# Kernel tuning notes

Hardware: AMD Instinct MI355X
Metric: run time of the kernel (lower is better)

## Reference

```python
import jax, jax.numpy as jnp
import numpy as np

B, T, C, H = 4, 2048, 1024, 16
HD = C // H  # head dim = 64


def setup_inputs() -> dict:
    key = jax.random.key(0)
    ks = jax.random.split(key, 8)
    s = 1.0 / np.sqrt(C)
    return {
        "x": jax.random.normal(ks[0], (B, T, C), dtype=jnp.float32),
        "Wq": jax.random.normal(ks[1], (C, C), dtype=jnp.float32) * s,
        "bq": jax.random.normal(ks[2], (C,), dtype=jnp.float32) * 0.02,
        "Wk": jax.random.normal(ks[3], (C, C), dtype=jnp.float32) * s,
        "bk": jax.random.normal(ks[4], (C,), dtype=jnp.float32) * 0.02,
        "Wv": jax.random.normal(ks[5], (C, C), dtype=jnp.float32) * s,
        "bv": jax.random.normal(ks[6], (C,), dtype=jnp.float32) * 0.02,
        "Wp": jax.random.normal(ks[7], (C, C), dtype=jnp.float32) * s,
    }


def reference(x, Wq, bq, Wk, bk, Wv, bv, Wp):
    # Separate Q/K/V projections (torch Linear: y = x @ W.T + b)
    q = jnp.einsum("btc,dc->btd", x, Wq) + bq
    k = jnp.einsum("btc,dc->btd", x, Wk) + bk
    v = jnp.einsum("btc,dc->btd", x, Wv) + bv
    # split heads -> [B, H, T, HD]
    q = q.reshape(B, T, H, HD).transpose(0, 2, 1, 3)
    k = k.reshape(B, T, H, HD).transpose(0, 2, 1, 3)
    v = v.reshape(B, T, H, HD).transpose(0, 2, 1, 3)
    # causal scaled dot-product attention
    scale = 1.0 / np.sqrt(HD)
    scores = jnp.einsum("bhqd,bhkd->bhqk", q, k) * scale
    causal_mask = jnp.tril(jnp.ones((T, T), dtype=bool))  # [T, T]
    scores = jnp.where(causal_mask, scores, jnp.finfo(scores.dtype).min)
    att = jax.nn.softmax(scores, axis=-1)
    y = jnp.einsum("bhqk,bhkd->bhqd", att, v)
    # merge heads and output projection (no bias)
    y = y.transpose(0, 2, 1, 3).reshape(B, T, C)
    return jnp.einsum("btc,dc->btd", y, Wp)
```

## Files before the change

kernel.cpp:

```cpp
#include <hip/hip_runtime.h>
#include <stdint.h>


typedef unsigned short u16;
typedef short bf16x8 __attribute__((ext_vector_type(8)));
typedef float f32x4  __attribute__((ext_vector_type(4)));

#define LOG2E 1.4426950408889634f
#define CSHIFT 8.0f

__device__ __forceinline__ void gload_lds16(const void* g, void* l) {
  __builtin_amdgcn_global_load_lds(
      (const __attribute__((address_space(1))) void*)g,
      (__attribute__((address_space(3))) void*)l,
      16, 0, 0);
}

__device__ __forceinline__ u16 f2bf(float f) {
  union { float f; uint32_t u; } v; v.f = f;
  uint32_t u = v.u;
  u += 0x7fffu + ((u >> 16) & 1u);
  return (u16)(u >> 16);
}

__device__ __forceinline__ uint32_t pack_bf16(float a, float b) {
#if __has_builtin(__builtin_amdgcn_cvt_pk_bf16_f32)
  typedef short v2s __attribute__((ext_vector_type(2)));
  v2s r = __builtin_amdgcn_cvt_pk_bf16_f32(a, b);
  union { v2s s; uint32_t u; } c; c.s = r;
  return c.u;
#else
  return (uint32_t)f2bf(a) | ((uint32_t)f2bf(b) << 16);
#endif
}

__device__ __forceinline__ float fexp2(float x) {
#if __has_builtin(__builtin_amdgcn_exp2f)
  return __builtin_amdgcn_exp2f(x);
#else
  return exp2f(x);
#endif
}

__device__ __forceinline__ float frcp(float x) {
#if __has_builtin(__builtin_amdgcn_rcpf)
  return __builtin_amdgcn_rcpf(x);
#else
  return 1.0f / x;
#endif
}

__global__ void cvt_all_kernel(const float* __restrict__ x,
                               const float* __restrict__ w0,
                               const float* __restrict__ w1,
                               const float* __restrict__ w2,
                               const float* __restrict__ w3,
                               uint4* __restrict__ out) {
  int i = blockIdx.x * blockDim.x + threadIdx.x;
  if (i >= 1572864) return;
  const float* src;
  int local;
  if (i < 1048576) { src = x; local = i; }
  else {
    int j = i - 1048576;
    int seg = j >> 17;
    local = j & 131071;
    src = (seg == 0) ? w0 : (seg == 1) ? w1 : (seg == 2) ? w2 : w3;
  }
  const int blk = local >> 9, s = local & 511;
  const int tile = blk >> 5, ks = blk & 31;
  const int r = s >> 6, ln = s & 63;
  const int row = tile * 128 + r * 16 + (ln & 15);
  const int col = ks * 32 + (ln >> 4) * 8;
  const float4* p = (const float4*)(src + (size_t)row * 1024 + col);
  const float4 v0 = p[0], v1 = p[1];
  uint4 pk;
  pk.x = pack_bf16(v0.x, v0.y); pk.y = pack_bf16(v0.z, v0.w);
  pk.z = pack_bf16(v1.x, v1.y); pk.w = pack_bf16(v1.z, v1.w);
  out[i] = pk;
}

__global__ __launch_bounds__(256, 3) void gemm_qkv(
    const u16* __restrict__ A,
    const u16* __restrict__ Wq, const u16* __restrict__ Wk, const u16* __restrict__ Wv,
    const float* __restrict__ bq, const float* __restrict__ bk, const float* __restrict__ bv,
    u16* __restrict__ Qo, u16* __restrict__ Ko, u16* __restrict__ Vo) {
  __shared__ __attribute__((aligned(16))) u16 shm[24576];
  const int tid = threadIdx.x;
  const int wv = tid >> 6, lane = tid & 63;
  const int cl = lane & 15, quad = lane >> 4;
  const int m0 = blockIdx.x * 128;
  const int mat = blockIdx.y >> 3;
  const int nt0 = blockIdx.y & 7;
  const int n0 = nt0 * 128;
  const int wm = (wv >> 1) * 64, wn = (wv & 1) * 64;
  const u16* W = (mat == 0) ? Wq : (mat == 1) ? Wk : Wv;
  const float* bias = (mat == 0) ? bq : (mat == 1) ? bk : bv;

  const u16* Abase = A + ((size_t)blockIdx.x << 17);
  const u16* Wbase = W + ((size_t)nt0 << 17);

  auto stage = [&](int buf, int ks) {
    const u16* a = Abase + ((size_t)ks << 12);
    const u16* w = Wbase + ((size_t)ks << 12);
    u16* la = &shm[buf * 4096];
    u16* lb = &shm[12288 + buf * 4096];
    gload_lds16(a + tid * 8,        la + tid * 8);
    gload_lds16(a + 2048 + tid * 8, la + 2048 + tid * 8);
    gload_lds16(w + tid * 8,        lb + tid * 8);
    gload_lds16(w + 2048 + tid * 8, lb + 2048 + tid * 8);
  };

  f32x4 acc[4][4] = {};

  stage(0, 0);
  stage(1, 1);

  for (int kt = 0; kt < 32; ++kt) {
    if (kt < 31) {
      asm volatile("s_waitcnt vmcnt(4)" ::: "memory");
    } else {
      asm volatile("s_waitcnt vmcnt(0)" ::: "memory");
    }
    __builtin_amdgcn_s_barrier();
    if (kt < 30) stage((kt + 2) % 3, kt + 2);
    const int buf = kt % 3;
    const u16* la = &shm[buf * 4096];
    const u16* lb = &shm[12288 + buf * 4096];
    bf16x8 af[4], bfr[4];
#pragma unroll
    for (int i = 0; i < 4; i++)
      af[i] = *(const bf16x8*)&la[(((wm >> 4) + i) * 64 + lane) * 8];
#pragma unroll
    for (int j = 0; j < 4; j++)
      bfr[j] = *(const bf16x8*)&lb[(((wn >> 4) + j) * 64 + lane) * 8];
#pragma unroll
    for (int i = 0; i < 4; i++)
#pragma unroll
      for (int j = 0; j < 4; j++)
        acc[i][j] = __builtin_amdgcn_mfma_f32_16x16x32_bf16(af[i], bfr[j], acc[i][j], 0, 0, 0);
  }

  __syncthreads();
  u16* etile = shm;

  if (mat == 2) {
#pragma unroll
    for (int j = 0; j < 4; j++) {
      const int n_loc = wn + j * 16 + cl;
      const float bj = bias[n0 + n_loc];
      const int hh = n_loc >> 6, hd = n_loc & 63;
#pragma unroll
      for (int i = 0; i < 4; i++) {
        const int tb = wm + i * 16 + quad * 4;
        uint2 pk;
        pk.x = pack_bf16(acc[i][j][0] + bj, acc[i][j][1] + bj);
        pk.y = pack_bf16(acc[i][j][2] + bj, acc[i][j][3] + bj);
        const int off = ((hd >> 4) * 4 + ((tb >> 5) & 3)) * 512
                      + (((tb >> 3) & 3) * 16 + (hd & 15)) * 8 + (tb & 7);
        *(uint2*)&etile[hh * 8192 + off] = pk;
      }
    }
  } else if (mat == 1) {
#pragma unroll
    for (int j = 0; j < 4; j++) {
      const int n_loc = wn + j * 16 + cl;
      const float bj = bias[n0 + n_loc];
      const int hh = n_loc >> 6, hd = n_loc & 63;
      const int rlo = hd >> 5, lhi = ((hd >> 3) & 3) * 16, e = hd & 7;
#pragma unroll
      for (int i = 0; i < 4; i++) {
#pragma unroll
        for (int r = 0; r < 4; r++) {
          const int tl = wm + i * 16 + quad * 4 + r;
          const int off = (((tl >> 4) & 7) * 2 + rlo) * 512 + (lhi + (tl & 15)) * 8 + e;
          etile[hh * 8192 + off] = f2bf(acc[i][j][r] + bj);
        }
      }
    }
  } else {
    const float sc = 0.125f * LOG2E;
#pragma unroll
    for (int j = 0; j < 4; j++) {
      const int n_loc = wn + j * 16 + cl;
      const float bj = bias[n0 + n_loc];
      const int hh = n_loc >> 6, hd = n_loc & 63;
#pragma unroll
      for (int i = 0; i < 4; i++) {
#pragma unroll
        for (int r = 0; r < 4; r++) {
          const int tl = wm + i * 16 + quad * 4 + r;
          etile[hh * 8192 + tl * 64 + hd] = f2bf((acc[i][j][r] + bj) * sc);
        }
      }
    }
  }
  __syncthreads();

  const int b = m0 >> 11, t0 = m0 & 2047;
  const int h0 = n0 >> 6;
  if (mat == 0) {
#pragma unroll
    for (int p = 0; p < 8; ++p) {
      const int idx = p * 2048 + tid * 8;
      const int hh = idx >> 13, off = idx & 8191;
      u16* dst = Qo + ((size_t)(b * 16 + h0 + hh) * 2048 + t0) * 64 + off;
      *(uint4*)dst = *(const uint4*)&etile[idx];
    }
  } else {
    u16* base = (mat == 1) ? Ko : Vo;
    const int kt = t0 >> 7;
#pragma unroll
    for (int p = 0; p < 8; ++p) {
      const int idx = p * 2048 + tid * 8;
      const int hh = idx >> 13, off = idx & 8191;
      u16* dst = base + ((size_t)(b * 16 + h0 + hh) << 17) + ((size_t)kt << 13) + off;
      *(uint4*)dst = *(const uint4*)&etile[idx];
    }
  }
}

__global__ __launch_bounds__(256, 3) void gemm_out(
    const u16* __restrict__ A, const u16* __restrict__ W,
    float* __restrict__ out) {
  __shared__ __attribute__((aligned(16))) u16 shm[24576];
  const int tid = threadIdx.x;
  const int wv = tid >> 6, lane = tid & 63;
  const int cl = lane & 15, quad = lane >> 4;
  const int m0 = blockIdx.x * 128;
  const int n0 = blockIdx.y * 128;
  const int wm = (wv >> 1) * 64, wn = (wv & 1) * 64;

  const u16* Abase = A + ((size_t)blockIdx.x << 17);
  const u16* Wbase = W + ((size_t)blockIdx.y << 17);

  auto stage = [&](int buf, int ks) {
    const u16* a = Abase + ((size_t)ks << 12);
    const u16* w = Wbase + ((size_t)ks << 12);
    u16* la = &shm[buf * 4096];
    u16* lb = &shm[12288 + buf * 4096];
    gload_lds16(a + tid * 8,        la + tid * 8);
    gload_lds16(a + 2048 + tid * 8, la + 2048 + tid * 8);
    gload_lds16(w + tid * 8,        lb + tid * 8);
    gload_lds16(w + 2048 + tid * 8, lb + 2048 + tid * 8);
  };

  f32x4 acc[4][4] = {};

  stage(0, 0);
  stage(1, 1);

  for (int kt = 0; kt < 32; ++kt) {
    if (kt < 31) {
      asm volatile("s_waitcnt vmcnt(4)" ::: "memory");
    } else {
      asm volatile("s_waitcnt vmcnt(0)" ::: "memory");
    }
    __builtin_amdgcn_s_barrier();
    if (kt < 30) stage((kt + 2) % 3, kt + 2);
    const int buf = kt % 3;
    const u16* la = &shm[buf * 4096];
    const u16* lb = &shm[12288 + buf * 4096];
    bf16x8 af[4], bfr[4];
#pragma unroll
    for (int i = 0; i < 4; i++)
      af[i] = *(const bf16x8*)&la[(((wm >> 4) + i) * 64 + lane) * 8];
#pragma unroll
    for (int j = 0; j < 4; j++)
      bfr[j] = *(const bf16x8*)&lb[(((wn >> 4) + j) * 64 + lane) * 8];
#pragma unroll
    for (int i = 0; i < 4; i++)
#pragma unroll
      for (int j = 0; j < 4; j++)
        acc[i][j] = __builtin_amdgcn_mfma_f32_16x16x32_bf16(af[i], bfr[j], acc[i][j], 0, 0, 0);
  }

  __syncthreads();
  float* etf = (float*)shm;
#pragma unroll
  for (int p = 0; p < 2; ++p) {
    if ((wm >> 6) == p) {
#pragma unroll
      for (int j = 0; j < 4; j++) {
        const int col = wn + j * 16 + cl;
#pragma unroll
        for (int i = 0; i < 4; i++)
#pragma unroll
          for (int r = 0; r < 4; r++) {
            const int row = i * 16 + quad * 4 + r;
            etf[row * 128 + col] = acc[i][j][r];
          }
      }
    }
    __syncthreads();
#pragma unroll
    for (int c = 0; c < 8; ++c) {
      const int lin4 = c * 256 + tid;
      const int fidx = lin4 * 4;
      const int row = fidx >> 7, col = fidx & 127;
      *(float4*)(out + (size_t)(m0 + p * 64 + row) * 1024 + n0 + col) =
          *(const float4*)&etf[fidx];
    }
    __syncthreads();
  }
}

__global__ __launch_bounds__(256, 2) void attn_kernel(
    const u16* __restrict__ Qb, const u16* __restrict__ Kb,
    const u16* __restrict__ Vtb, u16* __restrict__ Yb) {
  __shared__ __attribute__((aligned(16))) u16 ldsK[2][8192];
  __shared__ __attribute__((aligned(16))) u16 ldsV[8192];
  __shared__ __attribute__((aligned(16))) u16 ldsP[4][32][128];
  const int tid = threadIdx.x;
  const int wv = tid >> 6, lane = tid & 63;
  const int cl = lane & 15, quad = lane >> 4;
  const int p = blockIdx.x + (blockIdx.y << 3);
  const int xcd = p & 7, l = p >> 3;
  const int bh = xcd * 8 + (l & 7);
  const int qtb = l >> 3;
  const int qhi = 15 - qtb, qlo = qtb;
  const u16* Qh = Qb + (size_t)bh * 2048 * 64;
  const u16* Kh = Kb + ((size_t)bh << 17);
  const u16* Vh = Vtb + ((size_t)bh << 17);

  bf16x8 qf[2][2][2];
#pragma unroll
  for (int t = 0; t < 2; ++t) {
    const int q0 = (t == 0 ? qhi : qlo) * 128;
#pragma unroll
    for (int rt = 0; rt < 2; ++rt)
#pragma unroll
      for (int ks = 0; ks < 2; ++ks)
        qf[t][rt][ks] = *(const bf16x8*)&Qh[(size_t)(q0 + wv * 32 + rt * 16 + cl) * 64 + ks * 32 + quad * 8];
  }

  bf16x8 vone;
  {
    const short ob = (short)0x3F80;
#pragma unroll
    for (int e = 0; e < 8; ++e) vone[e] = (cl == 0) ? ob : (short)0;
  }

  f32x4 o[2][2][4] = {};
  f32x4 osum[2][2] = {};

  auto stageK = [&](int buf, int kt) {
    const u16* kb2 = Kh + ((size_t)kt << 13);
#pragma unroll
    for (int rep = 0; rep < 4; ++rep)
      gload_lds16(kb2 + (rep * 256 + tid) * 8, &ldsK[buf][(rep * 256 + tid) * 8]);
  };
  auto stageV = [&](int kt) {
    const u16* vb2 = Vh + ((size_t)kt << 13);
#pragma unroll
    for (int rep = 0; rep < 4; ++rep)
      gload_lds16(vb2 + (rep * 256 + tid) * 8, &ldsV[(rep * 256 + tid) * 8]);
  };

  stageK(0, 0);

  for (int kt = 0; kt <= qhi; ++kt) {
    const int buf = kt & 1;
    const bool dolo = (kt <= qlo);
    __syncthreads();

    stageV(kt);

#pragma unroll
    for (int ct = 0; ct < 8; ++ct) {
      const bf16x8 kf0 = *(const bf16x8*)&ldsK[buf][((ct * 2 + 0) * 64 + lane) * 8];
      const bf16x8 kf1 = *(const bf16x8*)&ldsK[buf][((ct * 2 + 1) * 64 + lane) * 8];
#pragma unroll
      for (int rt = 0; rt < 2; ++rt) {
        f32x4 s = {};
        s = __builtin_amdgcn_mfma_f32_16x16x32_bf16(kf0, qf[0][rt][0], s, 0, 0, 0);
        s = __builtin_amdgcn_mfma_f32_16x16x32_bf16(kf1, qf[0][rt][1], s, 0, 0, 0);
        float pv[4];
#pragma unroll
        for (int r = 0; r < 4; ++r) {
          pv[r] = fexp2(s[r] - CSHIFT);
          if (kt == qhi) {
            if (ct * 16 + quad * 4 + r > wv * 32 + rt * 16 + cl) pv[r] = 0.f;
          }
        }
        const int rl = rt * 16 + cl;
        const int swch = (2 * ct + (quad >> 1)) ^ (cl & 7);
        uint2 pw;
        pw.x = pack_bf16(pv[0], pv[1]);
        pw.y = pack_bf16(pv[2], pv[3]);
        *(uint2*)&ldsP[wv][rl][(swch << 3) + (quad & 1) * 4] = pw;
      }
    }

    __syncthreads();

    if (kt < qhi) stageK(1 - buf, kt + 1);

#pragma unroll
    for (int ks = 0; ks < 4; ++ks) {
      bf16x8 pf[2];
#pragma unroll
      for (int rt = 0; rt < 2; ++rt)
        pf[rt] = *(const bf16x8*)&ldsP[wv][rt * 16 + cl][(((4 * ks + quad) ^ (cl & 7)) << 3)];
#pragma unroll
      for (int nt = 0; nt < 4; ++nt) {
        const bf16x8 vf = *(const bf16x8*)&ldsV[((nt * 4 + ks) * 64 + lane) * 8];
        o[0][0][nt] = __builtin_amdgcn_mfma_f32_16x16x32_bf16(pf[0], vf, o[0][0][nt], 0, 0, 0);
        o[0][1][nt] = __builtin_amdgcn_mfma_f32_16x16x32_bf16(pf[1], vf, o[0][1][nt], 0, 0, 0);
      }
      osum[0][0] = __builtin_amdgcn_mfma_f32_16x16x32_bf16(pf[0], vone, osum[0][0], 0, 0, 0);
      osum[0][1] = __builtin_amdgcn_mfma_f32_16x16x32_bf16(pf[1], vone, osum[0][1], 0, 0, 0);
    }

    if (dolo) {
#pragma unroll
      for (int ct = 0; ct < 8; ++ct) {
        const bf16x8 kf0 = *(const bf16x8*)&ldsK[buf][((ct * 2 + 0) * 64 + lane) * 8];
        const bf16x8 kf1 = *(const bf16x8*)&ldsK[buf][((ct * 2 + 1) * 64 + lane) * 8];
#pragma unroll
        for (int rt = 0; rt < 2; ++rt) {
          f32x4 s = {};
          s = __builtin_amdgcn_mfma_f32_16x16x32_bf16(kf0, qf[1][rt][0], s, 0, 0, 0);
          s = __builtin_amdgcn_mfma_f32_16x16x32_bf16(kf1, qf[1][rt][1], s, 0, 0, 0);
          float pv[4];
#pragma unroll
          for (int r = 0; r < 4; ++r) {
            pv[r] = fexp2(s[r] - CSHIFT);
            if (kt == qlo) {
              if (ct * 16 + quad * 4 + r > wv * 32 + rt * 16 + cl) pv[r] = 0.f;
            }
          }
          const int rl = rt * 16 + cl;
          const int swch = (2 * ct + (quad >> 1)) ^ (cl & 7);
          uint2 pw;
          pw.x = pack_bf16(pv[0], pv[1]);
          pw.y = pack_bf16(pv[2], pv[3]);
          *(uint2*)&ldsP[wv][rl][(swch << 3) + (quad & 1) * 4] = pw;
        }
      }
#pragma unroll
      for (int ks = 0; ks < 4; ++ks) {
        bf16x8 pf[2];
#pragma unroll
        for (int rt = 0; rt < 2; ++rt)
          pf[rt] = *(const bf16x8*)&ldsP[wv][rt * 16 + cl][(((4 * ks + quad) ^ (cl & 7)) << 3)];
#pragma unroll
        for (int nt = 0; nt < 4; ++nt) {
          const bf16x8 vf = *(const bf16x8*)&ldsV[((nt * 4 + ks) * 64 + lane) * 8];
          o[1][0][nt] = __builtin_amdgcn_mfma_f32_16x16x32_bf16(pf[0], vf, o[1][0][nt], 0, 0, 0);
          o[1][1][nt] = __builtin_amdgcn_mfma_f32_16x16x32_bf16(pf[1], vf, o[1][1][nt], 0, 0, 0);
        }
        osum[1][0] = __builtin_amdgcn_mfma_f32_16x16x32_bf16(pf[0], vone, osum[1][0], 0, 0, 0);
        osum[1][1] = __builtin_amdgcn_mfma_f32_16x16x32_bf16(pf[1], vone, osum[1][1], 0, 0, 0);
      }
    }
  }

  const int bb = bh >> 4, h = bh & 15;
#pragma unroll
  for (int t = 0; t < 2; ++t) {
    const int q0 = (t == 0 ? qhi : qlo) * 128;
#pragma unroll
    for (int rt = 0; rt < 2; ++rt) {
#pragma unroll
      for (int r = 0; r < 4; ++r) {
        const float den = __shfl(osum[t][rt][r], quad << 4, 64);
        const float inv = frcp(den);
        const int q = q0 + wv * 32 + rt * 16 + quad * 4 + r;
        const int row = bb * 2048 + q;
#pragma unroll
        for (int nt = 0; nt < 4; ++nt) {
          const int col = h * 64 + nt * 16 + cl;
          const size_t off = ((size_t)((row >> 7) * 32 + (col >> 5)) << 12)
                           + (size_t)((((row >> 4) & 7) * 64 + ((col >> 3) & 3) * 16 + (row & 15)) * 8
                                      + (col & 7));
          Yb[off] = f2bf(o[t][rt][nt][r] * inv);
        }
      }
    }
  }
}

extern "C" void kernel_launch(void* const* d_in, const int* in_sizes, int n_in,
                              void* d_out, int out_size, void* d_ws, size_t ws_size,
                              hipStream_t stream) {
  const float* x  = (const float*)d_in[0];
  const float* Wq = (const float*)d_in[1];
  const float* bq = (const float*)d_in[2];
  const float* Wk = (const float*)d_in[3];
  const float* bk = (const float*)d_in[4];
  const float* Wv = (const float*)d_in[5];
  const float* bv = (const float*)d_in[6];
  const float* Wp = (const float*)d_in[7];

  u16* xb  = (u16*)d_ws;
  u16* wqb = xb  + 8388608;
  u16* wkb = wqb + 1048576;
  u16* wvb = wkb + 1048576;
  u16* wpb = wvb + 1048576;
  u16* Qb  = wpb + 1048576;
  u16* Kb  = Qb  + 8388608;
  u16* Vtb = Kb  + 8388608;
  u16* Yb  = Vtb + 8388608;

  cvt_all_kernel<<<6144, 256, 0, stream>>>(x, Wq, Wk, Wv, Wp, (uint4*)d_ws);

  gemm_qkv<<<dim3(64, 24), 256, 0, stream>>>(xb, wqb, wkb, wvb, bq, bk, bv,
                                             Qb, Kb, Vtb);

  attn_kernel<<<dim3(8, 64), 256, 0, stream>>>(Qb, Kb, Vtb, Yb);

  gemm_out<<<dim3(64, 8), 256, 0, stream>>>(Yb, wpb, (float*)d_out);
}
```

Baseline: 243.2 us.

## Coalesce bf16 conversion via LDS tiles and compute softmax row sums in registers

The fp32-to-bf16 conversion kernel now reads whole contiguous 16-row strips with coalesced float4 loads, stages the packed values in LDS, and writes them out in the swizzled MFMA tile layout, instead of each thread gathering scattered 32-byte pieces. In attention, the softmax denominator is accumulated as fp32 scalar adds per lane and reduced with cross-lane shuffles at the end, replacing the extra MFMA against a ones vector on every PV step. This removes matrix-core work and uncoalesced global reads, in exchange for more VALU adds, a block barrier in the conversion, and a full divide in place of the fast reciprocal.

```diff
diff --git a/kernel.cpp b/kernel.cpp
--- a/kernel.cpp
+++ b/kernel.cpp
@@ -42,42 +42,46 @@
 #endif
 }
 
-__device__ __forceinline__ float frcp(float x) {
-#if __has_builtin(__builtin_amdgcn_rcpf)
-  return __builtin_amdgcn_rcpf(x);
-#else
-  return 1.0f / x;
-#endif
-}
-
-__global__ void cvt_all_kernel(const float* __restrict__ x,
-                               const float* __restrict__ w0,
-                               const float* __restrict__ w1,
-                               const float* __restrict__ w2,
-                               const float* __restrict__ w3,
-                               uint4* __restrict__ out) {
-  int i = blockIdx.x * blockDim.x + threadIdx.x;
-  if (i >= 1572864) return;
+__global__ __launch_bounds__(256) void cvt_tile_kernel(
+    const float* __restrict__ x,
+    const float* __restrict__ w0, const float* __restrict__ w1,
+    const float* __restrict__ w2, const float* __restrict__ w3,
+    u16* __restrict__ ws) {
+  __shared__ __attribute__((aligned(16))) u16 lds[16][1032];
+  const int t = threadIdx.x;
+  const int rb = blockIdx.x;
   const float* src;
-  int local;
-  if (i < 1048576) { src = x; local = i; }
-  else {
-    int j = i - 1048576;
-    int seg = j >> 17;
-    local = j & 131071;
+  u16* dst;
+  int tile, r;
+  if (rb < 512) {
+    src = x; dst = ws; tile = rb >> 3; r = rb & 7;
+  } else {
+    const int j = rb - 512;
+    const int seg = j >> 6, local = j & 63;
     src = (seg == 0) ? w0 : (seg == 1) ? w1 : (seg == 2) ? w2 : w3;
-  }
-  const int blk = local >> 9, s = local & 511;
-  const int tile = blk >> 5, ks = blk & 31;
-  const int r = s >> 6, ln = s & 63;
-  const int row = tile * 128 + r * 16 + (ln & 15);
-  const int col = ks * 32 + (ln >> 4) * 8;
-  const float4* p = (const float4*)(src + (size_t)row * 1024 + col);
-  const float4 v0 = p[0], v1 = p[1];
-  uint4 pk;
-  pk.x = pack_bf16(v0.x, v0.y); pk.y = pack_bf16(v0.z, v0.w);
-  pk.z = pack_bf16(v1.x, v1.y); pk.w = pack_bf16(v1.z, v1.w);
-  out[i] = pk;
+    dst = ws + 8388608 + (size_t)seg * 1048576;
+    tile = local >> 3; r = local & 7;
+  }
+  const int row0 = tile * 128 + r * 16;
+
+#pragma unroll
+  for (int p2 = 0; p2 < 16; ++p2) {
+    const float4 v = *(const float4*)(src + (size_t)(row0 + p2) * 1024 + t * 4);
+    uint2 pk;
+    pk.x = pack_bf16(v.x, v.y);
+    pk.y = pack_bf16(v.z, v.w);
+    *(uint2*)&lds[p2][t * 4] = pk;
+  }
+  __syncthreads();
+
+  const int wv = t >> 6, ln = t & 63;
+  const int lr = ln & 15, lc = (ln >> 4) * 8;
+#pragma unroll
+  for (int k8 = 0; k8 < 8; ++k8) {
+    const int ks = k8 * 4 + wv;
+    const uint4 val = *(const uint4*)&lds[lr][ks * 32 + lc];
+    *(uint4*)(dst + ((((size_t)tile * 32 + ks) * 8 + r) * 64 + ln) * 8) = val;
+  }
 }
 
 __global__ __launch_bounds__(256, 3) void gemm_qkv(
@@ -334,15 +338,8 @@
         qf[t][rt][ks] = *(const bf16x8*)&Qh[(size_t)(q0 + wv * 32 + rt * 16 + cl) * 64 + ks * 32 + quad * 8];
   }
 
-  bf16x8 vone;
-  {
-    const short ob = (short)0x3F80;
-#pragma unroll
-    for (int e = 0; e < 8; ++e) vone[e] = (cl == 0) ? ob : (short)0;
-  }
-
   f32x4 o[2][2][4] = {};
-  f32x4 osum[2][2] = {};
+  float ls[2][2] = {};
 
   auto stageK = [&](int buf, int kt) {
     const u16* kb2 = Kh + ((size_t)kt << 13);
@@ -382,6 +379,7 @@
           if (kt == qhi) {
             if (ct * 16 + quad * 4 + r > wv * 32 + rt * 16 + cl) pv[r] = 0.f;
           }
+          ls[0][rt] += pv[r];
         }
         const int rl = rt * 16 + cl;
         const int swch = (2 * ct + (quad >> 1)) ^ (cl & 7);
@@ -408,8 +406,6 @@
         o[0][0][nt] = __builtin_amdgcn_mfma_f32_16x16x32_bf16(pf[0], vf, o[0][0][nt], 0, 0, 0);
         o[0][1][nt] = __builtin_amdgcn_mfma_f32_16x16x32_bf16(pf[1], vf, o[0][1][nt], 0, 0, 0);
       }
-      osum[0][0] = __builtin_amdgcn_mfma_f32_16x16x32_bf16(pf[0], vone, osum[0][0], 0, 0, 0);
-      osum[0][1] = __builtin_amdgcn_mfma_f32_16x16x32_bf16(pf[1], vone, osum[0][1], 0, 0, 0);
     }
 
     if (dolo) {
@@ -429,6 +425,7 @@
             if (kt == qlo) {
               if (ct * 16 + quad * 4 + r > wv * 32 + rt * 16 + cl) pv[r] = 0.f;
             }
+            ls[1][rt] += pv[r];
           }
           const int rl = rt * 16 + cl;
           const int swch = (2 * ct + (quad >> 1)) ^ (cl & 7);
@@ -450,8 +447,6 @@
           o[1][0][nt] = __builtin_amdgcn_mfma_f32_16x16x32_bf16(pf[0], vf, o[1][0][nt], 0, 0, 0);
           o[1][1][nt] = __builtin_amdgcn_mfma_f32_16x16x32_bf16(pf[1], vf, o[1][1][nt], 0, 0, 0);
         }
-        osum[1][0] = __builtin_amdgcn_mfma_f32_16x16x32_bf16(pf[0], vone, osum[1][0], 0, 0, 0);
-        osum[1][1] = __builtin_amdgcn_mfma_f32_16x16x32_bf16(pf[1], vone, osum[1][1], 0, 0, 0);
       }
     }
   }
@@ -462,10 +457,12 @@
     const int q0 = (t == 0 ? qhi : qlo) * 128;
 #pragma unroll
     for (int rt = 0; rt < 2; ++rt) {
+      float s = ls[t][rt];
+      s += __shfl_xor(s, 16, 64);
+      s += __shfl_xor(s, 32, 64);
 #pragma unroll
       for (int r = 0; r < 4; ++r) {
-        const float den = __shfl(osum[t][rt][r], quad << 4, 64);
-        const float inv = frcp(den);
+        const float inv = 1.0f / __shfl(s, quad * 4 + r, 64);
         const int q = q0 + wv * 32 + rt * 16 + quad * 4 + r;
         const int row = bb * 2048 + q;
 #pragma unroll
@@ -503,7 +500,7 @@
   u16* Vtb = Kb  + 8388608;
   u16* Yb  = Vtb + 8388608;
 
-  cvt_all_kernel<<<6144, 256, 0, stream>>>(x, Wq, Wk, Wv, Wp, (uint4*)d_ws);
+  cvt_tile_kernel<<<768, 256, 0, stream>>>(x, Wq, Wk, Wv, Wp, (u16*)d_ws);
 
   gemm_qkv<<<dim3(64, 24), 256, 0, stream>>>(xb, wqb, wkb, wvb, bq, bk, bv,
                                              Qb, Kb, Vtb);
```

Measured after the change: 233.4 us. 4.1% less time.
